# Kernel optimization log

Measured on AMD Instinct MI355X. Metric: run time of the kernel, lower is better.

Reference implementation:

```python
import jax, jax.numpy as jnp
import numpy as np

DIM = 256
NUM_HEADS = 8
HEAD_DIM = DIM // NUM_HEADS
CPB_HIDDEN = 512
B, N = 2, 2304
TABLE = 9025  # (2*48-1)**2


def _l2norm(t, eps=1e-12):
    # matches torch F.normalize(dim=-1): x / max(||x||, eps)
    n = jnp.sqrt(jnp.sum(t * t, axis=-1, keepdims=True))
    return t / jnp.maximum(n, eps)


def setup_inputs() -> dict:
    key = jax.random.key(0)
    ks = jax.random.split(key, 12)
    x = jax.random.normal(ks[0], (B, N, DIM), dtype=jnp.float32)
    relative_pos_index = jax.random.randint(ks[1], (N, N), 0, TABLE, dtype=jnp.int64)
    relative_coords_table = jax.random.uniform(ks[2], (TABLE, 2), dtype=jnp.float32) * 2.0 - 1.0
    seq_length_scale = jnp.ones((1,), dtype=jnp.float32) * jnp.log2(jnp.float32(N))
    padding_mask = jnp.zeros((B, N), dtype=jnp.int32)
    s = 0.02
    W_qkv = jax.random.normal(ks[3], (3 * DIM, DIM), dtype=jnp.float32) * s
    b_qkv = jnp.zeros((3 * DIM,), dtype=jnp.float32)
    # temperature init: log(exp(1/0.24) - 1) so softplus(temperature) = 1/0.24
    temperature = jnp.full((NUM_HEADS, 1, 1), float(np.log(np.expm1(1.0 / 0.24))), dtype=jnp.float32)
    query_embedding = jax.random.normal(ks[4], (NUM_HEADS, 1, HEAD_DIM), dtype=jnp.float32) * s
    W_proj = jax.random.normal(ks[5], (DIM, DIM), dtype=jnp.float32) * s
    b_proj = jnp.zeros((DIM,), dtype=jnp.float32)
    W_cpb1 = jax.random.normal(ks[6], (CPB_HIDDEN, 2), dtype=jnp.float32) * s
    b_cpb1 = jnp.zeros((CPB_HIDDEN,), dtype=jnp.float32)
    W_cpb2 = jax.random.normal(ks[7], (NUM_HEADS, CPB_HIDDEN), dtype=jnp.float32) * s
    b_cpb2 = jnp.zeros((NUM_HEADS,), dtype=jnp.float32)
    return {
        'x': x, 'relative_pos_index': relative_pos_index,
        'relative_coords_table': relative_coords_table,
        'seq_length_scale': seq_length_scale, 'padding_mask': padding_mask,
        'W_qkv': W_qkv, 'b_qkv': b_qkv, 'temperature': temperature,
        'query_embedding': query_embedding, 'W_proj': W_proj, 'b_proj': b_proj,
        'W_cpb1': W_cpb1, 'b_cpb1': b_cpb1, 'W_cpb2': W_cpb2, 'b_cpb2': b_cpb2,
    }


def reference(x, relative_pos_index, relative_coords_table, seq_length_scale,
              padding_mask, W_qkv, b_qkv, temperature, query_embedding,
              W_proj, b_proj, W_cpb1, b_cpb1, W_cpb2, b_cpb2):
    Bx, Nx, C = x.shape
    h, d = NUM_HEADS, HEAD_DIM
    # qkv projection -> (B, 3h, N, d); first h heads = q, then k, then v
    qkv = (jnp.einsum('bnc,oc->bno', x, W_qkv) + b_qkv)
    qkv = qkv.reshape(Bx, Nx, 3 * h, d).transpose(0, 2, 1, 3)
    q, k, v = qkv[:, :h], qkv[:, h:2 * h], qkv[:, 2 * h:]
    # CPB relative bias: (T,2) -> (T,h) -> (h,N,N) via gather
    hid = jax.nn.relu(relative_coords_table @ W_cpb1.T + b_cpb1)
    tab = hid @ W_cpb2.T + b_cpb2                    # (T, h)
    rel_bias = tab.T[:, relative_pos_index.reshape(-1)].reshape(h, Nx, Nx)
    # cosine-sim attention with learned query embedding + softplus temperature
    scale = jax.nn.softplus(temperature) * seq_length_scale[0]   # (h,1,1)
    qn = (_l2norm(q) + query_embedding) * scale                  # (B,h,N,d)
    kn = _l2norm(k)
    attn = jnp.einsum('bhnd,bhmd->bhnm', qn, kn) + rel_bias
    attn = jax.nn.softmax(attn, axis=-1)
    out = jnp.einsum('bhnm,bhmd->bhnd', attn, v)
    out = out.transpose(0, 2, 1, 3).reshape(Bx, Nx, C)
    out = out @ W_proj.T + b_proj
    return out
```

## Files before the change

kernel.cpp:

```cpp
#include <hip/hip_runtime.h>
#include <math.h>

#define DIMC 256
#define NHEADS 8
#define HDIM 32
#define CPBH 512
#define BB 2
#define NSEQ 2304
#define TAB 9025
#define TABP 9040
#define RTOT (BB*NHEADS*NSEQ)
#define SPLITS 4
#define MSP (NSEQ/SPLITS)
#define PBS 36
#define NCHUNK (NSEQ/32)
#define LOG2E 1.44269504088896340736f

#define NWQ (3*DIMC*DIMC)
#define IDXP_ELEMS    (NSEQ * NCHUNK * 16)
#define IDXP4_BLOCKS  (IDXP_ELEMS / 1024)
#define CPB_BLOCKS    ((TAB + 63) / 64)
#define QKV_BLOCKS    (12 * 72)

typedef unsigned short ushort;
typedef __attribute__((ext_vector_type(8))) short short8;
typedef __attribute__((ext_vector_type(4))) short short4v;
typedef __attribute__((ext_vector_type(4))) float f32x4;

#define MFMA16(a,b,c) __builtin_amdgcn_mfma_f32_16x16x32_bf16((a),(b),(c),0,0,0)

__device__ __forceinline__ ushort f2bf(float x) {
  unsigned u = __float_as_uint(x);
  u += 0x7FFFu + ((u >> 16) & 1u);
  return (ushort)(u >> 16);
}
__device__ __forceinline__ float bf2f(ushort b) {
  return __uint_as_float(((unsigned)b) << 16);
}
__device__ __forceinline__ float fexp2(float x) {
#if defined(__has_builtin)
#if __has_builtin(__builtin_amdgcn_exp2f)
  return __builtin_amdgcn_exp2f(x);
#else
  return exp2f(x);
#endif
#else
  return exp2f(x);
#endif
}
__device__ __forceinline__ unsigned pack_trunc(float p0, float p1) {
  return __builtin_amdgcn_perm(__float_as_uint(p1), __float_as_uint(p0), 0x07060302u);
}
__device__ __forceinline__ void cvt8(const float* __restrict__ p, short8* hi, short8* lo) {
  float4 v0 = *(const float4*)p;
  float4 v1 = *(const float4*)(p + 4);
  float vv[8] = {v0.x, v0.y, v0.z, v0.w, v1.x, v1.y, v1.z, v1.w};
  short8 h, l;
#pragma unroll
  for (int i = 0; i < 8; ++i) {
    ushort hh = f2bf(vv[i]);
    h[i] = (short)hh;
    l[i] = (short)f2bf(vv[i] - bf2f(hh));
  }
  *hi = h; *lo = l;
}

__launch_bounds__(256)
__global__ void pre_kernel(const float* __restrict__ x, const float* __restrict__ wq,
                           const int* __restrict__ idx,
                           const float* __restrict__ tbl, const float* __restrict__ W1,
                           const float* __restrict__ b1, const float* __restrict__ W2,
                           const float* __restrict__ b2,
                           const float* __restrict__ bias, const float* __restrict__ temp,
                           const float* __restrict__ sls, const float* __restrict__ qe,
                           ushort* __restrict__ qhi, ushort* __restrict__ qlo,
                           ushort* __restrict__ khi, ushort* __restrict__ klo,
                           ushort* __restrict__ vT,
                           unsigned* __restrict__ idxP, ushort* __restrict__ tabBf) {
  __shared__ __align__(16) float smem[8192];
  int blk = blockIdx.x;
  int tid = threadIdx.x;

  if (blk < CPB_BLOCKS) {
    float* w1b = smem;
    float* w2t = smem + 2048;
    float* part = smem + 6144;
    for (int i = tid; i < CPBH; i += 256) {
      w1b[i * 4 + 0] = W1[2 * i];
      w1b[i * 4 + 1] = W1[2 * i + 1];
      w1b[i * 4 + 2] = b1[i];
      w1b[i * 4 + 3] = 0.f;
    }
    for (int i = tid; i < CPBH * NHEADS; i += 256)
      w2t[(i & (CPBH - 1)) * NHEADS + (i >> 9)] = W2[i];
    int tl = tid & 63, jc = tid >> 6;
    int t = blk * 64 + tl;
    bool valid = t < TAB;
    float c0 = 0.f, c1 = 0.f;
    if (valid) { c0 = tbl[2 * t]; c1 = tbl[2 * t + 1]; }
    __syncthreads();
    float acc[NHEADS];
#pragma unroll
    for (int h = 0; h < NHEADS; ++h) acc[h] = 0.f;
    for (int j = jc * 128; j < jc * 128 + 128; ++j) {
      float4 wv = *(const float4*)&w1b[j * 4];
      float hid = fmaxf(fmaf(c0, wv.x, fmaf(c1, wv.y, wv.z)), 0.f);
      float4 wa = *(const float4*)&w2t[j * NHEADS];
      float4 wb = *(const float4*)&w2t[j * NHEADS + 4];
      acc[0] = fmaf(hid, wa.x, acc[0]);
      acc[1] = fmaf(hid, wa.y, acc[1]);
      acc[2] = fmaf(hid, wa.z, acc[2]);
      acc[3] = fmaf(hid, wa.w, acc[3]);
      acc[4] = fmaf(hid, wb.x, acc[4]);
      acc[5] = fmaf(hid, wb.y, acc[5]);
      acc[6] = fmaf(hid, wb.z, acc[6]);
      acc[7] = fmaf(hid, wb.w, acc[7]);
    }
#pragma unroll
    for (int h = 0; h < NHEADS; ++h) part[((size_t)jc * 64 + tl) * NHEADS + h] = acc[h];
    __syncthreads();
    if (jc == 0 && valid) {
#pragma unroll
      for (int h = 0; h < NHEADS; ++h) {
        float s = b2[h];
#pragma unroll
        for (int p = 0; p < 4; ++p) s += part[((size_t)p * 64 + tl) * NHEADS + h];
        tabBf[h * TABP + t] = f2bf(s * LOG2E);
      }
    }
  } else if (blk < CPB_BLOCKS + QKV_BLOCKS) {
    float (*vbuf)[65] = (float(*)[65])smem;
    int t = blk - CPB_BLOCKS;
    int n0 = (t % 12) * 64, m0 = (t / 12) * 64;
    int lane = tid & 63, w = tid >> 6;
    int g = lane >> 4, c = lane & 15;
    int mw = m0 + w * 16;
    const int K = DIMC;
    f32x4 acc[4] = {{0,0,0,0},{0,0,0,0},{0,0,0,0},{0,0,0,0}};
#pragma unroll 2
    for (int k0 = 0; k0 < K; k0 += 32) {
      short8 ah, al;
      cvt8(&x[(size_t)(mw + c) * K + k0 + g * 8], &ah, &al);
#pragma unroll
      for (int nt = 0; nt < 4; ++nt) {
        short8 bh, bl;
        cvt8(&wq[(size_t)(n0 + nt * 16 + c) * K + k0 + g * 8], &bh, &bl);
        acc[nt] = MFMA16(ah, bh, acc[nt]);
        acc[nt] = MFMA16(al, bh, acc[nt]);
        acc[nt] = MFMA16(ah, bl, acc[nt]);
      }
    }
#pragma unroll
    for (int nt = 0; nt < 4; ++nt) {
      float bv = bias[n0 + nt * 16 + c];
#pragma unroll
      for (int r = 0; r < 4; ++r) acc[nt][r] += bv;
    }

    int b = (m0 >= NSEQ) ? 1 : 0;
    int nb = m0 - b * NSEQ;
    int sect = n0 >> 8;
    int hloc = (n0 & 255) >> 5;

    if (sect < 2) {
#pragma unroll
      for (int H = 0; H < 2; ++H) {
        int head = hloc + H;
        float scale = (sect == 0) ? log1pf(expf(temp[head])) * sls[0] * LOG2E : 0.f;
#pragma unroll
        for (int r = 0; r < 4; ++r) {
          float ss = acc[2*H][r]*acc[2*H][r] + acc[2*H+1][r]*acc[2*H+1][r];
          ss += __shfl_xor(ss, 1);
          ss += __shfl_xor(ss, 2);
          ss += __shfl_xor(ss, 4);
          ss += __shfl_xor(ss, 8);
          float inv = 1.f / fmaxf(sqrtf(ss), 1e-12f);
#pragma unroll
          for (int half = 0; half < 2; ++half) {
            int d = half * 16 + c;
            float val = acc[2*H + half][r] * inv;
            if (sect == 0) val = (val + qe[head * HDIM + d]) * scale;
            vbuf[w * 16 + g * 4 + r][H * 32 + d] = val;
          }
        }
      }
      __syncthreads();
      int plane = tid >> 7;
      int seg = tid & 127;
      int head = seg >> 6, row = seg & 63;
      const float* srcrow = &vbuf[row][head * 32];
      ushort out16[32];
#pragma unroll
      for (int i = 0; i < 32; ++i) {
        float v = srcrow[i];
        ushort hh = f2bf(v);
        out16[i] = plane ? f2bf(v - bf2f(hh)) : hh;
      }
      ushort* dstp = plane ? (sect == 0 ? qlo : klo) : (sect == 0 ? qhi : khi);
      size_t off = ((size_t)(b * NHEADS + hloc + head) * NSEQ + nb + row) * HDIM;
#pragma unroll
      for (int q4 = 0; q4 < 4; ++q4)
        *(int4*)&dstp[off + q4 * 8] = ((int4*)out16)[q4];
    } else {
#pragma unroll
      for (int nt = 0; nt < 4; ++nt)
#pragma unroll
        for (int r = 0; r < 4; ++r)
          vbuf[w * 16 + g * 4 + r][nt * 16 + c] = acc[nt][r];
      __syncthreads();
      int hbase = (n0 - 512) >> 5;
#pragma unroll
      for (int it = 0; it < 16; ++it) {
        int dloc = (tid >> 6) * 16 + it;
        int p = tid & 63;
        int pp = p & 31;
        int nsrc = (p & 32) + (pp & 1) * 16 + (pp >> 1);
        float v = vbuf[nsrc][dloc];
        int head = hbase + (dloc >> 5), d = dloc & 31;
        vT[((size_t)((b * NHEADS + head) * HDIM + d)) * NSEQ + nb + p] = f2bf(v);
      }
    }
  } else {
    int t4 = (blk - CPB_BLOCKS - QKV_BLOCKS) * 256 + tid;
    int cc4 = (t4 & 3) * 4;
    int ch = (t4 >> 2) % NCHUNK;
    int n = t4 / (4 * NCHUNK);
    int mbase = ch * 32 + cc4;
    int4 a = *(const int4*)&idx[(size_t)n * NSEQ + mbase];
    int4 b = *(const int4*)&idx[(size_t)n * NSEQ + mbase + 16];
    uint4 o;
    o.x = (unsigned)a.x | ((unsigned)b.x << 16);
    o.y = (unsigned)a.y | ((unsigned)b.y << 16);
    o.z = (unsigned)a.z | ((unsigned)b.z << 16);
    o.w = (unsigned)a.w | ((unsigned)b.w << 16);
    *(uint4*)&idxP[((size_t)n * NCHUNK + ch) * 16 + cc4] = o;
  }
}

__launch_bounds__(256)
__global__ void attn_kernel(const ushort* __restrict__ qhi, const ushort* __restrict__ qlo,
                            const ushort* __restrict__ khi, const ushort* __restrict__ klo,
                            const ushort* __restrict__ vT, const ushort* __restrict__ tabBf,
                            const unsigned* __restrict__ idxP,
                            float* __restrict__ pO, float* __restrict__ pL) {
  __shared__ ushort tbf[10240];
  __shared__ __align__(16) ushort pbuf[8][16 * PBS];
  int tid = threadIdx.x;
  int lane = tid & 63;
  int w = tid >> 6;
  int qb = blockIdx.x;
  int by = blockIdx.y;
  int s = by & 3, bh = by >> 2;
  int h = bh & (NHEADS - 1);

  const ushort* tsrc = tabBf + h * TABP;
#pragma unroll
  for (int i = 0; i < 5; ++i) {
    int off = i * 2048 + tid * 8;
    *(int4*)&tbf[off] = *(const int4*)&tsrc[off];
  }

  int g = lane >> 4, c = lane & 15;
  int q0 = qb * 128 + w * 16;
  int q1 = q0 + 64;
  size_t rowbase = (size_t)bh * NSEQ;

  short8 qAh = *(const short8*)&qhi[(rowbase + q0 + c) * HDIM + g * 8];
  short8 qAl = *(const short8*)&qlo[(rowbase + q0 + c) * HDIM + g * 8];
  short8 qBh = *(const short8*)&qhi[(rowbase + q1 + c) * HDIM + g * 8];
  short8 qBl = *(const short8*)&qlo[(rowbase + q1 + c) * HDIM + g * 8];
  __syncthreads();

  short one = (c == 0) ? (short)0x3F80 : (short)0;
  short8 onesB = {one, one, one, one, one, one, one, one};

  f32x4 oa0 = {0,0,0,0}, oa1 = {0,0,0,0}, ob0 = {0,0,0,0}, ob1 = {0,0,0,0};
  f32x4 la = {0,0,0,0}, lb = {0,0,0,0};
  ushort* pba = pbuf[w * 2];
  ushort* pbb = pbuf[w * 2 + 1];
  int m0 = s * MSP;

#define LOADK(MT, D0H, D0L, D1H, D1L, IA0, IA1, IA2, IA3, IB0, IB1, IB2, IB3) do { \
    size_t ra_ = (rowbase + (MT) + c) * HDIM + g * 8;                 \
    D0H = *(const short8*)&khi[ra_];                                  \
    D0L = *(const short8*)&klo[ra_];                                  \
    D1H = *(const short8*)&khi[ra_ + 16 * HDIM];                      \
    D1L = *(const short8*)&klo[ra_ + 16 * HDIM];                      \
    size_t ia_ = ((size_t)(q0 + g * 4) * NCHUNK + ((MT) >> 5)) * 16 + c; \
    IA0 = idxP[ia_];                                                  \
    IA1 = idxP[ia_ + (size_t)NCHUNK * 16];                            \
    IA2 = idxP[ia_ + (size_t)2 * NCHUNK * 16];                        \
    IA3 = idxP[ia_ + (size_t)3 * NCHUNK * 16];                        \
    size_t ibx_ = ((size_t)(q1 + g * 4) * NCHUNK + ((MT) >> 5)) * 16 + c; \
    IB0 = idxP[ibx_];                                                 \
    IB1 = idxP[ibx_ + (size_t)NCHUNK * 16];                           \
    IB2 = idxP[ibx_ + (size_t)2 * NCHUNK * 16];                       \
    IB3 = idxP[ibx_ + (size_t)3 * NCHUNK * 16];                       \
  } while (0)

  short8 c0h, c0l, c1h, c1l;
  unsigned ia0, ia1, ia2, ia3, ib0, ib1, ib2, ib3;
  LOADK(m0, c0h, c0l, c1h, c1l, ia0, ia1, ia2, ia3, ib0, ib1, ib2, ib3);

  for (int mt = m0; mt < m0 + MSP; mt += 32) {
    int mtn = (mt + 32 < m0 + MSP) ? (mt + 32) : m0;
    short8 n0h, n0l, n1h, n1l;
    unsigned ja0, ja1, ja2, ja3, jb0, jb1, jb2, jb3;
    LOADK(mtn, n0h, n0l, n1h, n1l, ja0, ja1, ja2, ja3, jb0, jb1, jb2, jb3);

    f32x4 sa0 = {0,0,0,0}, sa1 = {0,0,0,0}, sb0 = {0,0,0,0}, sb1 = {0,0,0,0};
    sa0 = MFMA16(qAh, c0h, sa0);
    sb0 = MFMA16(qBh, c0h, sb0);
    sa1 = MFMA16(qAh, c1h, sa1);
    sb1 = MFMA16(qBh, c1h, sb1);
    sa0 = MFMA16(qAl, c0h, sa0);
    sb0 = MFMA16(qBl, c0h, sb0);
    sa1 = MFMA16(qAl, c1h, sa1);
    sb1 = MFMA16(qBl, c1h, sb1);
    sa0 = MFMA16(qAh, c0l, sa0);
    sb0 = MFMA16(qBh, c0l, sb0);
    sa1 = MFMA16(qAh, c1l, sa1);
    sb1 = MFMA16(qBh, c1l, sb1);

    size_t va = ((size_t)(bh * HDIM + c)) * NSEQ + mt + g * 8;
    short8 vf0 = *(const short8*)&vT[va];
    short8 vf1 = *(const short8*)&vT[va + 16 * NSEQ];

    unsigned ipa[4] = {ia0, ia1, ia2, ia3};
    unsigned ipb[4] = {ib0, ib1, ib2, ib3};
#pragma unroll
    for (int r = 0; r < 4; ++r) {
      int k0 = ipa[r] & 0xFFFF, k1 = ipa[r] >> 16;
      float pA0 = fexp2(sa0[r] + bf2f(tbf[k0]));
      float pA1 = fexp2(sa1[r] + bf2f(tbf[k1]));
      *(unsigned*)&pba[(g * 4 + r) * PBS + 2 * c] = pack_trunc(pA0, pA1);
    }
#pragma unroll
    for (int r = 0; r < 4; ++r) {
      int k0 = ipb[r] & 0xFFFF, k1 = ipb[r] >> 16;
      float pB0 = fexp2(sb0[r] + bf2f(tbf[k0]));
      float pB1 = fexp2(sb1[r] + bf2f(tbf[k1]));
      *(unsigned*)&pbb[(g * 4 + r) * PBS + 2 * c] = pack_trunc(pB0, pB1);
    }

    short4v paA = *(const short4v*)&pba[c * PBS + g * 8];
    short4v paB = *(const short4v*)&pba[c * PBS + g * 8 + 4];
    short8 pfa = __builtin_shufflevector(paA, paB, 0, 1, 2, 3, 4, 5, 6, 7);
    short4v pbA = *(const short4v*)&pbb[c * PBS + g * 8];
    short4v pbB = *(const short4v*)&pbb[c * PBS + g * 8 + 4];
    short8 pfb = __builtin_shufflevector(pbA, pbB, 0, 1, 2, 3, 4, 5, 6, 7);

    oa0 = MFMA16(pfa, vf0, oa0);
    oa1 = MFMA16(pfa, vf1, oa1);
    ob0 = MFMA16(pfb, vf0, ob0);
    ob1 = MFMA16(pfb, vf1, ob1);
    la  = MFMA16(pfa, onesB, la);
    lb  = MFMA16(pfb, onesB, lb);

    c0h = n0h; c0l = n0l; c1h = n1h; c1l = n1l;
    ia0 = ja0; ia1 = ja1; ia2 = ja2; ia3 = ja3;
    ib0 = jb0; ib1 = jb1; ib2 = jb2; ib3 = jb3;
  }
#undef LOADK

  size_t prow0 = (size_t)s * RTOT + rowbase;
#pragma unroll
  for (int r = 0; r < 4; ++r) {
    size_t pra = prow0 + q0 + g * 4 + r;
    pO[pra * HDIM + c]      = oa0[r];
    pO[pra * HDIM + 16 + c] = oa1[r];
    size_t prb = prow0 + q1 + g * 4 + r;
    pO[prb * HDIM + c]      = ob0[r];
    pO[prb * HDIM + 16 + c] = ob1[r];
    if (c == 0) { pL[pra] = la[r]; pL[prb] = lb[r]; }
  }
}

#define ALD 264
__launch_bounds__(256)
__global__ void gemm_proj_fused(const float* __restrict__ pO, const float* __restrict__ pL,
                                const float* __restrict__ Wp,
                                const float* __restrict__ bias, float* __restrict__ C) {
  __shared__ __align__(16) ushort Ahs[64 * ALD];
  __shared__ __align__(16) ushort Als[64 * ALD];
  int tid = threadIdx.x;
  int m0 = blockIdx.x * 64;
  int b = (m0 >= NSEQ) ? 1 : 0;
  int nb = m0 - b * NSEQ;

  {
    int r = tid >> 2;
    int q = tid & 3;
    int n = nb + r;
#pragma unroll
    for (int h = 0; h < NHEADS; ++h) {
      size_t bhn = (size_t)(b * NHEADS + h) * NSEQ + n;
      float L = 0.f;
#pragma unroll
      for (int sp = 0; sp < SPLITS; ++sp) L += pL[(size_t)sp * RTOT + bhn];
      float inv = 1.f / L;
      float a[8] = {0.f, 0.f, 0.f, 0.f, 0.f, 0.f, 0.f, 0.f};
#pragma unroll
      for (int sp = 0; sp < SPLITS; ++sp) {
        const float* src = &pO[((size_t)sp * RTOT + bhn) * HDIM + q * 8];
        float4 v0 = *(const float4*)&src[0];
        float4 v1 = *(const float4*)&src[4];
        a[0] += v0.x; a[1] += v0.y; a[2] += v0.z; a[3] += v0.w;
        a[4] += v1.x; a[5] += v1.y; a[6] += v1.z; a[7] += v1.w;
      }
      ushort hi8[8], lo8[8];
#pragma unroll
      for (int i = 0; i < 8; ++i) {
        float v = a[i] * inv;
        ushort hh = f2bf(v);
        hi8[i] = hh;
        lo8[i] = f2bf(v - bf2f(hh));
      }
      int k = h * 32 + q * 8;
      *(int4*)&Ahs[r * ALD + k] = *(int4*)hi8;
      *(int4*)&Als[r * ALD + k] = *(int4*)lo8;
    }
  }
  __syncthreads();

  int lane = tid & 63, w = tid >> 6;
  int g = lane >> 4, c = lane & 15;
  int n0 = w * 64;
  f32x4 acc[4][4] = {};
  for (int k0 = 0; k0 < DIMC; k0 += 32) {
    short8 bfh[4], bfl[4];
#pragma unroll
    for (int nt = 0; nt < 4; ++nt)
      cvt8(&Wp[(size_t)(n0 + nt * 16 + c) * DIMC + k0 + g * 8], &bfh[nt], &bfl[nt]);
#pragma unroll
    for (int mt = 0; mt < 4; ++mt) {
      short8 ah = *(const short8*)&Ahs[(mt * 16 + c) * ALD + k0 + g * 8];
      short8 al = *(const short8*)&Als[(mt * 16 + c) * ALD + k0 + g * 8];
#pragma unroll
      for (int nt = 0; nt < 4; ++nt) {
        acc[mt][nt] = MFMA16(ah, bfh[nt], acc[mt][nt]);
        acc[mt][nt] = MFMA16(al, bfh[nt], acc[mt][nt]);
        acc[mt][nt] = MFMA16(ah, bfl[nt], acc[mt][nt]);
      }
    }
  }
#pragma unroll
  for (int nt = 0; nt < 4; ++nt) {
    float bv = bias[n0 + nt * 16 + c];
#pragma unroll
    for (int mt = 0; mt < 4; ++mt)
#pragma unroll
      for (int r = 0; r < 4; ++r)
        C[(size_t)(m0 + mt * 16 + g * 4 + r) * DIMC + n0 + nt * 16 + c] = acc[mt][nt][r] + bv;
  }
}

extern "C" void kernel_launch(void* const* d_in, const int* in_sizes, int n_in,
                              void* d_out, int out_size, void* d_ws, size_t ws_size,
                              hipStream_t stream) {
  const float* x    = (const float*)d_in[0];
  const int*   idx  = (const int*)d_in[1];
  const float* tbl  = (const float*)d_in[2];
  const float* sls  = (const float*)d_in[3];
  const float* Wqkv = (const float*)d_in[5];
  const float* bqkv = (const float*)d_in[6];
  const float* temp = (const float*)d_in[7];
  const float* qe   = (const float*)d_in[8];
  const float* Wp   = (const float*)d_in[9];
  const float* bp   = (const float*)d_in[10];
  const float* W1   = (const float*)d_in[11];
  const float* b1   = (const float*)d_in[12];
  const float* W2   = (const float*)d_in[13];
  const float* b2   = (const float*)d_in[14];

  float* ws   = (float*)d_ws;
  float* pO   = ws;
  float* pL   = pO + (size_t)SPLITS * RTOT * HDIM;
  unsigned* idxP = (unsigned*)(pL + (size_t)SPLITS * RTOT);
  ushort* u   = (ushort*)(idxP + IDXP_ELEMS);
  ushort* qhi = u;                u += (size_t)RTOT * HDIM;
  ushort* qlo = u;                u += (size_t)RTOT * HDIM;
  ushort* khi = u;                u += (size_t)RTOT * HDIM;
  ushort* klo = u;                u += (size_t)RTOT * HDIM;
  ushort* vT  = u;                u += (size_t)RTOT * HDIM;
  ushort* tabBf = u;              u += 73728;
  float* out  = (float*)d_out;

  pre_kernel<<<dim3(CPB_BLOCKS + QKV_BLOCKS + IDXP4_BLOCKS), dim3(256), 0, stream>>>(
      x, Wqkv, idx, tbl, W1, b1, W2, b2, bqkv, temp, sls, qe,
      qhi, qlo, khi, klo, vT, idxP, tabBf);
  attn_kernel<<<dim3(NSEQ / 128, BB * NHEADS * SPLITS), dim3(256), 0, stream>>>(
      qhi, qlo, khi, klo, vT, tabBf, idxP, pO, pL);
  gemm_proj_fused<<<dim3((BB * NSEQ) / 64), dim3(256), 0, stream>>>(
      pO, pL, Wp, bp, out);
}
```

Before: 214.1 us.

## Repack relative-index layout for vector loads, prefetch V, add MFMA priority hints

Changes the packed index layout so that each lane's four rows of packed bias indices are contiguous, letting the attention kernel fetch them with one 16-byte load per q-block instead of four scalar loads. V fragments are now prefetched one tile ahead together with K, so their load latency is hidden behind the current iteration. s_setprio raises wave priority around the MFMA sections so the matrix instructions are issued ahead of other waves. The cost is more live registers for the extra prefetch, and the repack now does uncoalesced scalar reads of idx.

```diff
diff --git a/kernel.cpp b/kernel.cpp
--- a/kernel.cpp
+++ b/kernel.cpp
@@ -222,18 +222,18 @@
     }
   } else {
     int t4 = (blk - CPB_BLOCKS - QKV_BLOCKS) * 256 + tid;
-    int cc4 = (t4 & 3) * 4;
-    int ch = (t4 >> 2) % NCHUNK;
-    int n = t4 / (4 * NCHUNK);
-    int mbase = ch * 32 + cc4;
-    int4 a = *(const int4*)&idx[(size_t)n * NSEQ + mbase];
-    int4 b = *(const int4*)&idx[(size_t)n * NSEQ + mbase + 16];
-    uint4 o;
-    o.x = (unsigned)a.x | ((unsigned)b.x << 16);
-    o.y = (unsigned)a.y | ((unsigned)b.y << 16);
-    o.z = (unsigned)a.z | ((unsigned)b.z << 16);
-    o.w = (unsigned)a.w | ((unsigned)b.w << 16);
-    *(uint4*)&idxP[((size_t)n * NCHUNK + ch) * 16 + cc4] = o;
+    int grp = t4 >> 4;
+    int ch = grp % NCHUNK;
+    int n4 = grp / NCHUNK;
+    int m = ch * 32 + (t4 & 15);
+    unsigned o[4];
+#pragma unroll
+    for (int i = 0; i < 4; ++i) {
+      unsigned lo = (unsigned)idx[(size_t)(n4 * 4 + i) * NSEQ + m];
+      unsigned hi = (unsigned)idx[(size_t)(n4 * 4 + i) * NSEQ + m + 16];
+      o[i] = lo | (hi << 16);
+    }
+    *(uint4*)&idxP[(size_t)t4 * 4] = *(const uint4*)o;
   }
 }
 
@@ -263,6 +263,7 @@
   int g = lane >> 4, c = lane & 15;
   int q0 = qb * 128 + w * 16;
   int q1 = q0 + 64;
+  int qg0 = q0 >> 2, qg1 = q1 >> 2;
   size_t rowbase = (size_t)bh * NSEQ;
 
   short8 qAh = *(const short8*)&qhi[(rowbase + q0 + c) * HDIM + g * 8];
@@ -280,35 +281,37 @@
   ushort* pbb = pbuf[w * 2 + 1];
   int m0 = s * MSP;
 
-#define LOADK(MT, D0H, D0L, D1H, D1L, IA0, IA1, IA2, IA3, IB0, IB1, IB2, IB3) do { \
+#define LOADK(MT, D0H, D0L, D1H, D1L, IA, IB) do {                    \
     size_t ra_ = (rowbase + (MT) + c) * HDIM + g * 8;                 \
     D0H = *(const short8*)&khi[ra_];                                  \
     D0L = *(const short8*)&klo[ra_];                                  \
     D1H = *(const short8*)&khi[ra_ + 16 * HDIM];                      \
     D1L = *(const short8*)&klo[ra_ + 16 * HDIM];                      \
-    size_t ia_ = ((size_t)(q0 + g * 4) * NCHUNK + ((MT) >> 5)) * 16 + c; \
-    IA0 = idxP[ia_];                                                  \
-    IA1 = idxP[ia_ + (size_t)NCHUNK * 16];                            \
-    IA2 = idxP[ia_ + (size_t)2 * NCHUNK * 16];                        \
-    IA3 = idxP[ia_ + (size_t)3 * NCHUNK * 16];                        \
-    size_t ibx_ = ((size_t)(q1 + g * 4) * NCHUNK + ((MT) >> 5)) * 16 + c; \
-    IB0 = idxP[ibx_];                                                 \
-    IB1 = idxP[ibx_ + (size_t)NCHUNK * 16];                           \
-    IB2 = idxP[ibx_ + (size_t)2 * NCHUNK * 16];                       \
-    IB3 = idxP[ibx_ + (size_t)3 * NCHUNK * 16];                       \
+    size_t ia_ = ((size_t)(qg0 + g) * NCHUNK + ((MT) >> 5)) * 64 + c * 4; \
+    IA = *(const uint4*)&idxP[ia_];                                   \
+    size_t ib_ = ((size_t)(qg1 + g) * NCHUNK + ((MT) >> 5)) * 64 + c * 4; \
+    IB = *(const uint4*)&idxP[ib_];                                   \
   } while (0)
-
-  short8 c0h, c0l, c1h, c1l;
-  unsigned ia0, ia1, ia2, ia3, ib0, ib1, ib2, ib3;
-  LOADK(m0, c0h, c0l, c1h, c1l, ia0, ia1, ia2, ia3, ib0, ib1, ib2, ib3);
+#define LOADV(MT, V0, V1) do {                                        \
+    size_t va_ = ((size_t)(bh * HDIM + c)) * NSEQ + (MT) + g * 8;     \
+    V0 = *(const short8*)&vT[va_];                                    \
+    V1 = *(const short8*)&vT[va_ + 16 * NSEQ];                        \
+  } while (0)
+
+  short8 c0h, c0l, c1h, c1l, vf0, vf1;
+  uint4 ia, ib;
+  LOADK(m0, c0h, c0l, c1h, c1l, ia, ib);
+  LOADV(m0, vf0, vf1);
 
   for (int mt = m0; mt < m0 + MSP; mt += 32) {
     int mtn = (mt + 32 < m0 + MSP) ? (mt + 32) : m0;
-    short8 n0h, n0l, n1h, n1l;
-    unsigned ja0, ja1, ja2, ja3, jb0, jb1, jb2, jb3;
-    LOADK(mtn, n0h, n0l, n1h, n1l, ja0, ja1, ja2, ja3, jb0, jb1, jb2, jb3);
+    short8 n0h, n0l, n1h, n1l, u0, u1;
+    uint4 ja, jb;
+    LOADK(mtn, n0h, n0l, n1h, n1l, ja, jb);
+    LOADV(mtn, u0, u1);
 
     f32x4 sa0 = {0,0,0,0}, sa1 = {0,0,0,0}, sb0 = {0,0,0,0}, sb1 = {0,0,0,0};
+    __builtin_amdgcn_s_setprio(1);
     sa0 = MFMA16(qAh, c0h, sa0);
     sb0 = MFMA16(qBh, c0h, sb0);
     sa1 = MFMA16(qAh, c1h, sa1);
@@ -321,13 +324,10 @@
     sb0 = MFMA16(qBh, c0l, sb0);
     sa1 = MFMA16(qAh, c1l, sa1);
     sb1 = MFMA16(qBh, c1l, sb1);
-
-    size_t va = ((size_t)(bh * HDIM + c)) * NSEQ + mt + g * 8;
-    short8 vf0 = *(const short8*)&vT[va];
-    short8 vf1 = *(const short8*)&vT[va + 16 * NSEQ];
-
-    unsigned ipa[4] = {ia0, ia1, ia2, ia3};
-    unsigned ipb[4] = {ib0, ib1, ib2, ib3};
+    __builtin_amdgcn_s_setprio(0);
+
+    unsigned ipa[4] = {ia.x, ia.y, ia.z, ia.w};
+    unsigned ipb[4] = {ib.x, ib.y, ib.z, ib.w};
 #pragma unroll
     for (int r = 0; r < 4; ++r) {
       int k0 = ipa[r] & 0xFFFF, k1 = ipa[r] >> 16;
@@ -350,18 +350,21 @@
     short4v pbB = *(const short4v*)&pbb[c * PBS + g * 8 + 4];
     short8 pfb = __builtin_shufflevector(pbA, pbB, 0, 1, 2, 3, 4, 5, 6, 7);
 
+    __builtin_amdgcn_s_setprio(1);
     oa0 = MFMA16(pfa, vf0, oa0);
     oa1 = MFMA16(pfa, vf1, oa1);
     ob0 = MFMA16(pfb, vf0, ob0);
     ob1 = MFMA16(pfb, vf1, ob1);
     la  = MFMA16(pfa, onesB, la);
     lb  = MFMA16(pfb, onesB, lb);
+    __builtin_amdgcn_s_setprio(0);
 
     c0h = n0h; c0l = n0l; c1h = n1h; c1l = n1l;
-    ia0 = ja0; ia1 = ja1; ia2 = ja2; ia3 = ja3;
-    ib0 = jb0; ib1 = jb1; ib2 = jb2; ib3 = jb3;
+    vf0 = u0; vf1 = u1;
+    ia = ja; ib = jb;
   }
 #undef LOADK
+#undef LOADV
 
   size_t prow0 = (size_t)s * RTOT + rowbase;
 #pragma unroll
```

Measured after the change: 214.5 us. Within noise of the previous version (+0.1%).
